# Kernel tuning notes

Measured on AMD Instinct MI355X. Metric: run time of the kernel, lower is better.

The kernel has to match this reference:

```python
import jax, jax.numpy as jnp
import numpy as np

D = 1024      # d_model
H = 8         # heads
DH = D // H
L = 12        # layers
E = 4         # experts
F = 2048      # dim_feedforward
NCLS = 10
SPARSITY = 0.5
EPS = 1e-5
B, S = 4, 512


def _xavier(key, shape):
    fan_in, fan_out = shape[-1], shape[-2] if len(shape) > 1 else shape[-1]
    scale = jnp.sqrt(2.0 / (fan_in + fan_out))
    return jax.random.normal(key, shape, jnp.float32) * scale


def setup_inputs() -> dict:
    key = jax.random.key(0)
    ks = jax.random.split(key, 16)
    return {
        "x": jax.random.normal(ks[0], (B, S, D), jnp.float32),
        "pos": jax.random.normal(ks[1], (1, 512, D), jnp.float32) * 0.02,
        # stacked per-layer transformer params
        "Wqkv": _xavier(ks[2], (L, 3 * D, D)), "bqkv": jnp.zeros((L, 3 * D), jnp.float32),
        "Wo": _xavier(ks[3], (L, D, D)),       "bo": jnp.zeros((L, D), jnp.float32),
        "ln1_s": jnp.ones((L, D), jnp.float32), "ln1_b": jnp.zeros((L, D), jnp.float32),
        "W1": _xavier(ks[4], (L, F, D)), "b1": jnp.zeros((L, F), jnp.float32),
        "W2": _xavier(ks[5], (L, D, F)), "b2": jnp.zeros((L, D), jnp.float32),
        "ln2_s": jnp.ones((L, D), jnp.float32), "ln2_b": jnp.zeros((L, D), jnp.float32),
        # shared gate / experts / classifier
        "Wg": _xavier(ks[6], (E, D)), "bg": jnp.zeros((E,), jnp.float32),
        "We": _xavier(ks[7], (E, D, D)), "be": jnp.zeros((E, D), jnp.float32),
        "Wf": _xavier(ks[8], (NCLS, D)), "bf": jnp.zeros((NCLS,), jnp.float32),
    }


def _layernorm(x, s, b):
    m = jnp.mean(x, axis=-1, keepdims=True)
    v = jnp.mean(jnp.square(x - m), axis=-1, keepdims=True)
    return (x - m) * jax.lax.rsqrt(v + EPS) * s + b


def _forward(x, pos, Wqkv, bqkv, Wo, bo, ln1_s, ln1_b, W1, b1, W2, b2,
             ln2_s, ln2_b, Wg, bg, We, be, Wf, bf):
    Bx, Sx, _ = x.shape
    x = x + pos[:, :Sx, :]
    for l in range(L):
        # --- self-attention (post-norm TransformerEncoderLayer, eval/no-dropout) ---
        qkv = x @ Wqkv[l].T + bqkv[l]                      # [B,S,3D]
        q, k, v = jnp.split(qkv, 3, axis=-1)
        q = q.reshape(Bx, Sx, H, DH).transpose(0, 2, 1, 3)  # bhsd
        k = k.reshape(Bx, Sx, H, DH).transpose(0, 2, 1, 3)
        v = v.reshape(Bx, Sx, H, DH).transpose(0, 2, 1, 3)
        attn = jax.nn.softmax(jnp.einsum('bhqd,bhkd->bhqk', q, k) / jnp.sqrt(jnp.float32(DH)), axis=-1)
        o = jnp.einsum('bhqk,bhkd->bhqd', attn, v).transpose(0, 2, 1, 3).reshape(Bx, Sx, D)
        o = o @ Wo[l].T + bo[l]
        x = _layernorm(x + o, ln1_s[l], ln1_b[l])
        # --- ffn (exact gelu) ---
        h = jax.nn.gelu(x @ W1[l].T + b1[l], approximate=False) @ W2[l].T + b2[l]
        x = _layernorm(x + h, ln2_s[l], ln2_b[l])
        # --- top-2 gated MoE (shared gate/experts across layers) ---
        gs = jax.nn.softmax(x @ Wg.T + bg, axis=-1)         # [B,S,E]
        vals, idx = jax.lax.top_k(gs, 2)                    # [B,S,2]
        all_out = jnp.einsum('bsd,eod->bseo', x, We) + be   # [B,S,E,D]
        sel = jnp.take_along_axis(all_out, idx[..., None], axis=2)  # [B,S,2,D]
        expert_out = jnp.sum(sel * vals[..., None], axis=2)
        x = x * (1.0 - SPARSITY) + expert_out * SPARSITY
    return x[:, -1, :] @ Wf.T + bf                          # [B,10]


def reference(x, pos, Wqkv, bqkv, Wo, bo, ln1_s, ln1_b, W1, b1, W2, b2,
              ln2_s, ln2_b, Wg, bg, We, be, Wf, bf):
    return _forward(x, pos, Wqkv, bqkv, Wo, bo, ln1_s, ln1_b, W1, b1, W2, b2,
                    ln2_s, ln2_b, Wg, bg, We, be, Wf, bf)
```

## Files before the change

### kernel.cpp

```cpp
#include <hip/hip_runtime.h>
#include <math.h>

#define D     1024
#define NH    8
#define DHD   128
#define NL    12
#define NE    4
#define FF    2048
#define NCLS  10
#define BB    4
#define SS    512
#define TT    (BB*SS)
#define EPSV  1e-5f
#define SPARS 0.5f

typedef __attribute__((ext_vector_type(8))) short bf16x8;
typedef __attribute__((ext_vector_type(4))) float f32x4;
typedef unsigned short ushortT;

__device__ __forceinline__ ushortT f2bf(float f) {
    unsigned u = __float_as_uint(f);
    u += 0x7FFF + ((u >> 16) & 1);
    return (ushortT)(u >> 16);
}
__device__ __forceinline__ float bf2f(ushortT h) {
    return __uint_as_float(((unsigned)h) << 16);
}

#define LDP 40

template<int MODE, int SK, int ACT, int BN>
__global__ __launch_bounds__(256)
void gemm_mfma(const ushortT* __restrict__ A, const float* __restrict__ Bw,
               const float* __restrict__ bias, void* __restrict__ Cv,
               int M, int N, int Ktot, int Klen, long eBw, long eBias, long eC)
{
    const int z = blockIdx.z;
    int koff = 0;
    float* Cf = nullptr; ushortT* Ch = nullptr;
    if constexpr (SK > 1) {
        koff = z * Klen;
        Cf = (float*)Cv + (size_t)z * M * N;
    } else {
        Bw   += (size_t)z * eBw;
        bias += (size_t)z * eBias;
        if constexpr (MODE == 0) Ch = (ushortT*)Cv + (size_t)z * eC;
        else                     Cf = (float*)Cv   + (size_t)z * eC;
    }

    constexpr int MR = (BN == 128) ? 4 : 2;
    __shared__ ushortT Asl[128 * LDP];
    __shared__ ushortT Bsl[BN * LDP];

    const int tid  = threadIdx.x;
    const int wave = tid >> 6, lane = tid & 63;
    const int wm = (BN == 128) ? (wave >> 1) * 64 : wave * 32;
    const int wn = (BN == 128) ? (wave & 1) * 64 : 0;
    const int fr = lane & 15;
    const int fq = lane >> 4;

    const int m0 = blockIdx.y * 128;
    const int n0 = blockIdx.x * BN;

    const int arow = tid >> 1;
    const int akc  = (tid & 1) * 2;
    const ushortT* Ag = A + (size_t)(m0 + arow) * Ktot + koff;
    const int srow = (BN == 128) ? (tid >> 3) : (tid >> 2);
    const int scb  = (BN == 128) ? (tid & 7) : (tid & 3);
    const float* Bg = Bw + (size_t)(n0 + srow) * Ktot + koff + scb * 4;

    f32x4 acc[MR][4] = {};

    for (int k0 = 0; k0 < Klen; k0 += 32) {
        bf16x8 av8[2];
        float4 bv[4];
        #pragma unroll
        for (int u = 0; u < 2; ++u)
            av8[u] = *reinterpret_cast<const bf16x8*>(Ag + k0 + (akc + u) * 8);
        if constexpr (BN == 128) {
            #pragma unroll
            for (int p = 0; p < 4; ++p)
                bv[p] = *reinterpret_cast<const float4*>(Bg + (size_t)(32*p) * Ktot + k0);
        } else {
            bv[0] = *reinterpret_cast<const float4*>(Bg + k0);
            bv[1] = *reinterpret_cast<const float4*>(Bg + k0 + 16);
        }
        __syncthreads();
        #pragma unroll
        for (int u = 0; u < 2; ++u)
            *reinterpret_cast<bf16x8*>(&Asl[arow*LDP + (akc + u)*8]) = av8[u];
        if constexpr (BN == 128) {
            #pragma unroll
            for (int p = 0; p < 4; ++p) {
                ushort4 b4; b4.x=f2bf(bv[p].x); b4.y=f2bf(bv[p].y); b4.z=f2bf(bv[p].z); b4.w=f2bf(bv[p].w);
                *reinterpret_cast<ushort4*>(&Bsl[(srow + 32*p)*LDP + scb*4]) = b4;
            }
        } else {
            ushort4 b0; b0.x=f2bf(bv[0].x); b0.y=f2bf(bv[0].y); b0.z=f2bf(bv[0].z); b0.w=f2bf(bv[0].w);
            ushort4 b1; b1.x=f2bf(bv[1].x); b1.y=f2bf(bv[1].y); b1.z=f2bf(bv[1].z); b1.w=f2bf(bv[1].w);
            *reinterpret_cast<ushort4*>(&Bsl[srow*LDP + scb*4])      = b0;
            *reinterpret_cast<ushort4*>(&Bsl[srow*LDP + scb*4 + 16]) = b1;
        }
        __syncthreads();

        bf16x8 af[MR], bfr[4];
        #pragma unroll
        for (int i = 0; i < MR; ++i)
            af[i]  = *reinterpret_cast<const bf16x8*>(&Asl[(wm + i*16 + fr)*LDP + fq*8]);
        #pragma unroll
        for (int j = 0; j < 4; ++j)
            bfr[j] = *reinterpret_cast<const bf16x8*>(&Bsl[(wn + j*16 + fr)*LDP + fq*8]);
        #pragma unroll
        for (int i = 0; i < MR; ++i)
            #pragma unroll
            for (int j = 0; j < 4; ++j)
                acc[i][j] = __builtin_amdgcn_mfma_f32_16x16x32_bf16(af[i], bfr[j], acc[i][j], 0, 0, 0);
    }

    #pragma unroll
    for (int j = 0; j < 4; ++j) {
        const int n = n0 + wn + j*16 + fr;
        float bb = 0.f;
        if constexpr (SK == 1) bb = bias[n];
        #pragma unroll
        for (int i = 0; i < MR; ++i) {
            const int mb = m0 + wm + i*16 + fq*4;
            if constexpr (SK > 1) {
                #pragma unroll
                for (int r = 0; r < 4; ++r)
                    Cf[(size_t)(mb + r) * N + n] = acc[i][j][r];
            } else if constexpr (MODE == 0) {
                #pragma unroll
                for (int r = 0; r < 4; ++r) {
                    float u = acc[i][j][r] + bb;
                    if constexpr (ACT == 1) u = 0.5f*u*(1.0f + erff(u*0.70710678118654752f));
                    Ch[(size_t)(mb + r) * N + n] = f2bf(u);
                }
            } else {
                #pragma unroll
                for (int r = 0; r < 4; ++r) {
                    float u = acc[i][j][r] + bb;
                    if constexpr (ACT == 1) u = 0.5f*u*(1.0f + erff(u*0.70710678118654752f));
                    Cf[(size_t)(mb + r) * N + n] = u;
                }
            }
        }
    }
}

__global__ __launch_bounds__(256)
void kv_prep(const float* __restrict__ qkv, ushortT* __restrict__ Kb, ushortT* __restrict__ Vt)
{
    __shared__ ushortT T[64*136];
    const int tid = threadIdx.x;
    const int st = blockIdx.x, bh = blockIdx.y;
    const int b = bh >> 3, h = bh & 7;
    const float* base = qkv + (size_t)(b*SS + st*64)*3*D + h*DHD;

    #pragma unroll
    for (int p = 0; p < 4; ++p) {
        const int row = (tid >> 4) + 16*p;
        const int colb = (tid & 15) * 8;
        {
            const float* src = base + (size_t)row*3*D + D + colb;
            float f[8];
            *reinterpret_cast<float4*>(f)   = *reinterpret_cast<const float4*>(src);
            *reinterpret_cast<float4*>(f+4) = *reinterpret_cast<const float4*>(src+4);
            bf16x8 u;
            #pragma unroll
            for (int e = 0; e < 8; ++e) ((ushortT*)&u)[e] = f2bf(f[e]);
            *reinterpret_cast<bf16x8*>(&Kb[((size_t)bh*SS + st*64 + row)*DHD + colb]) = u;
        }
        {
            const float* src = base + (size_t)row*3*D + 2*D + colb;
            float f[8];
            *reinterpret_cast<float4*>(f)   = *reinterpret_cast<const float4*>(src);
            *reinterpret_cast<float4*>(f+4) = *reinterpret_cast<const float4*>(src+4);
            #pragma unroll
            for (int e = 0; e < 8; ++e) T[row*136 + colb + e] = f2bf(f[e]);
        }
    }
    __syncthreads();
    #pragma unroll
    for (int p = 0; p < 4; ++p) {
        const int d  = (tid >> 3) + 32*p;
        const int sb = (tid & 7) * 8;
        bf16x8 u;
        #pragma unroll
        for (int e = 0; e < 8; ++e) ((ushortT*)&u)[e] = T[(sb + e)*136 + d];
        *reinterpret_cast<bf16x8*>(&Vt[((size_t)bh*DHD + d)*SS + st*64 + sb]) = u;
    }
}

#define KLP 136
#define VLP 72
#define PLP 72

__global__ __launch_bounds__(256)
void attn_mfma(const float* __restrict__ qkv, const ushortT* __restrict__ Kb,
               const ushortT* __restrict__ Vt, ushortT* __restrict__ o16)
{
    __shared__ ushortT Kl[64*KLP];
    __shared__ ushortT Vl[128*VLP];
    __shared__ ushortT Pl[4*16*PLP];

    const int tid = threadIdx.x;
    const int w = tid >> 6, lane = tid & 63;
    const int g = lane >> 4, c = lane & 15;
    const int bh = blockIdx.y;
    const int b = bh >> 3, h = bh & 7;
    const int q0 = blockIdx.x*64 + w*16;
    ushortT* Pw = Pl + w*16*PLP;

    bf16x8 qhi[4], qlo[4];
    const float scale = 0.08838834764831845f;
    {
        const float* Qrow = qkv + (size_t)(b*SS + q0 + c)*3*D + h*DHD;
        #pragma unroll
        for (int db = 0; db < 4; ++db) {
            float f[8];
            *reinterpret_cast<float4*>(f)   = *reinterpret_cast<const float4*>(Qrow + db*32 + g*8);
            *reinterpret_cast<float4*>(f+4) = *reinterpret_cast<const float4*>(Qrow + db*32 + g*8 + 4);
            #pragma unroll
            for (int e = 0; e < 8; ++e) {
                const float fs = f[e]*scale;
                const ushortT hi = f2bf(fs);
                ((ushortT*)&qhi[db])[e] = hi;
                ((ushortT*)&qlo[db])[e] = f2bf(fs - bf2f(hi));
            }
        }
    }

    const ushortT* Kg = Kb + (size_t)bh*SS*DHD;
    const ushortT* Vg = Vt + (size_t)bh*DHD*SS;

    float m_r[4], l_r[4];
    #pragma unroll
    for (int r = 0; r < 4; ++r) { m_r[r] = -1e30f; l_r[r] = 0.f; }
    f32x4 oacc[8] = {};

    for (int kt = 0; kt < SS/64; ++kt) {
        __syncthreads();
        #pragma unroll
        for (int p = 0; p < 4; ++p) {
            const int row = (tid >> 4) + 16*p;
            const int colb = (tid & 15)*8;
            bf16x8 u = *reinterpret_cast<const bf16x8*>(&Kg[(size_t)(kt*64 + row)*DHD + colb]);
            *reinterpret_cast<bf16x8*>(&Kl[row*KLP + colb]) = u;
        }
        #pragma unroll
        for (int p = 0; p < 4; ++p) {
            const int dr = (tid >> 3) + 32*p;
            const int sb = (tid & 7)*8;
            bf16x8 u = *reinterpret_cast<const bf16x8*>(&Vg[(size_t)dr*SS + kt*64 + sb]);
            *reinterpret_cast<bf16x8*>(&Vl[dr*VLP + sb]) = u;
        }
        __syncthreads();

        f32x4 s[4] = {};
        #pragma unroll
        for (int db = 0; db < 4; ++db) {
            bf16x8 kf[4];
            #pragma unroll
            for (int kb = 0; kb < 4; ++kb)
                kf[kb] = *reinterpret_cast<const bf16x8*>(&Kl[(kb*16 + c)*KLP + db*32 + g*8]);
            #pragma unroll
            for (int kb = 0; kb < 4; ++kb) {
                s[kb] = __builtin_amdgcn_mfma_f32_16x16x32_bf16(qhi[db], kf[kb], s[kb], 0, 0, 0);
                s[kb] = __builtin_amdgcn_mfma_f32_16x16x32_bf16(qlo[db], kf[kb], s[kb], 0, 0, 0);
            }
        }

        float tmax[4];
        #pragma unroll
        for (int r = 0; r < 4; ++r)
            tmax[r] = fmaxf(fmaxf(s[0][r], s[1][r]), fmaxf(s[2][r], s[3][r]));
        #pragma unroll
        for (int off = 1; off < 16; off <<= 1)
            #pragma unroll
            for (int r = 0; r < 4; ++r)
                tmax[r] = fmaxf(tmax[r], __shfl_xor(tmax[r], off));
        float mn[4], corr[4];
        #pragma unroll
        for (int r = 0; r < 4; ++r) {
            mn[r] = fmaxf(m_r[r], tmax[r]);
            corr[r] = __expf(m_r[r] - mn[r]);
            m_r[r] = mn[r];
        }
        float tsum[4] = {0.f, 0.f, 0.f, 0.f};
        #pragma unroll
        for (int kb = 0; kb < 4; ++kb)
            #pragma unroll
            for (int r = 0; r < 4; ++r) {
                const float p = __expf(s[kb][r] - mn[r]);
                s[kb][r] = p;
                tsum[r] += p;
            }
        #pragma unroll
        for (int off = 1; off < 16; off <<= 1)
            #pragma unroll
            for (int r = 0; r < 4; ++r)
                tsum[r] += __shfl_xor(tsum[r], off);
        #pragma unroll
        for (int r = 0; r < 4; ++r) l_r[r] = l_r[r]*corr[r] + tsum[r];
        #pragma unroll
        for (int df = 0; df < 8; ++df)
            #pragma unroll
            for (int r = 0; r < 4; ++r)
                oacc[df][r] *= corr[r];

        #pragma unroll
        for (int kb = 0; kb < 4; ++kb)
            #pragma unroll
            for (int r = 0; r < 4; ++r)
                Pw[(g*4 + r)*PLP + kb*16 + c] = f2bf(s[kb][r]);

        #pragma unroll
        for (int kk = 0; kk < 2; ++kk) {
            bf16x8 pa = *reinterpret_cast<const bf16x8*>(&Pw[c*PLP + kk*32 + g*8]);
            #pragma unroll
            for (int df = 0; df < 8; ++df) {
                bf16x8 vb = *reinterpret_cast<const bf16x8*>(&Vl[(df*16 + c)*VLP + kk*32 + g*8]);
                oacc[df] = __builtin_amdgcn_mfma_f32_16x16x32_bf16(pa, vb, oacc[df], 0, 0, 0);
            }
        }
    }

    #pragma unroll
    for (int r = 0; r < 4; ++r) {
        const float inv = 1.0f / l_r[r];
        ushortT* orow = o16 + (size_t)(b*SS + q0 + g*4 + r)*D + h*DHD + c;
        #pragma unroll
        for (int df = 0; df < 8; ++df)
            orow[df*16] = f2bf(oacc[df][r] * inv);
    }
}

template<int SK, int GATE>
__global__ __launch_bounds__(256)
void add_ln_r(const float* __restrict__ xin, const float* __restrict__ P,
              const float* __restrict__ dbias,
              const float* __restrict__ gs, const float* __restrict__ gb,
              float* __restrict__ x32, ushortT* __restrict__ x16,
              const float* __restrict__ Wg, const float* __restrict__ bg,
              float* __restrict__ gv, int* __restrict__ gi)
{
    const int row = blockIdx.x, tid = threadIdx.x;
    const size_t off = (size_t)row*D + tid*4;
    float4 a = *reinterpret_cast<const float4*>(xin + off);
    float d0, d1, d2, d3;
    {
        float4 bvd = *reinterpret_cast<const float4*>(dbias + tid*4);
        d0 = bvd.x; d1 = bvd.y; d2 = bvd.z; d3 = bvd.w;
    }
    #pragma unroll
    for (int s = 0; s < SK; ++s) {
        float4 pv = *reinterpret_cast<const float4*>(P + (size_t)s*TT*D + off);
        d0 += pv.x; d1 += pv.y; d2 += pv.z; d3 += pv.w;
    }
    float v0=a.x+d0, v1=a.y+d1, v2=a.z+d2, v3=a.w+d3;
    __shared__ float red[2][4];
    float s = v0+v1+v2+v3;
    #pragma unroll
    for (int o = 32; o; o >>= 1) s += __shfl_xor(s, o, 64);
    if ((tid & 63) == 0) red[0][tid>>6] = s;
    __syncthreads();
    const float mean = (red[0][0]+red[0][1]+red[0][2]+red[0][3]) * (1.0f/D);
    v0-=mean; v1-=mean; v2-=mean; v3-=mean;
    float qv = v0*v0+v1*v1+v2*v2+v3*v3;
    #pragma unroll
    for (int o = 32; o; o >>= 1) qv += __shfl_xor(qv, o, 64);
    if ((tid & 63) == 0) red[1][tid>>6] = qv;
    __syncthreads();
    const float var = (red[1][0]+red[1][1]+red[1][2]+red[1][3]) * (1.0f/D);
    const float rstd = rsqrtf(var + EPSV);
    float4 sv = *reinterpret_cast<const float4*>(gs + tid*4);
    float4 bv = *reinterpret_cast<const float4*>(gb + tid*4);
    float ov[4];
    ov[0] = v0*rstd*sv.x + bv.x;
    ov[1] = v1*rstd*sv.y + bv.y;
    ov[2] = v2*rstd*sv.z + bv.z;
    ov[3] = v3*rstd*sv.w + bv.w;
    float4 o4; o4.x=ov[0]; o4.y=ov[1]; o4.z=ov[2]; o4.w=ov[3];
    *reinterpret_cast<float4*>(x32 + off) = o4;
    ushort4 h4; h4.x=f2bf(ov[0]); h4.y=f2bf(ov[1]); h4.z=f2bf(ov[2]); h4.w=f2bf(ov[3]);
    *reinterpret_cast<ushort4*>(x16 + off) = h4;

    if constexpr (GATE) {
        float p[4] = {0.f, 0.f, 0.f, 0.f};
        #pragma unroll
        for (int e = 0; e < 4; ++e) {
            const float* wr = Wg + (size_t)e*D + tid*4;
            p[e] = ov[0]*wr[0] + ov[1]*wr[1] + ov[2]*wr[2] + ov[3]*wr[3];
        }
        #pragma unroll
        for (int o = 32; o; o >>= 1) {
            p[0] += __shfl_xor(p[0], o, 64); p[1] += __shfl_xor(p[1], o, 64);
            p[2] += __shfl_xor(p[2], o, 64); p[3] += __shfl_xor(p[3], o, 64);
        }
        __shared__ float gred[4][4];
        if ((tid & 63) == 0) {
            const int w = tid>>6;
            gred[w][0]=p[0]; gred[w][1]=p[1]; gred[w][2]=p[2]; gred[w][3]=p[3];
        }
        __syncthreads();
        if (tid == 0) {
            float g[4];
            #pragma unroll
            for (int e = 0; e < 4; ++e) g[e] = gred[0][e]+gred[1][e]+gred[2][e]+gred[3][e] + bg[e];
            const float mx = fmaxf(fmaxf(g[0],g[1]), fmaxf(g[2],g[3]));
            float ssum = 0.f;
            #pragma unroll
            for (int e = 0; e < 4; ++e) { g[e] = __expf(g[e]-mx); ssum += g[e]; }
            const float inv = 1.0f/ssum;
            #pragma unroll
            for (int e = 0; e < 4; ++e) g[e] *= inv;
            int i0 = 0;
            for (int e = 1; e < 4; ++e) if (g[e] > g[i0]) i0 = e;
            int i1 = (i0 == 0) ? 1 : 0;
            for (int e = 0; e < 4; ++e) if (e != i0 && g[e] > g[i1]) i1 = e;
            gv[row*2]   = g[i0]; gv[row*2+1] = g[i1];
            gi[row*2]   = i0;    gi[row*2+1] = i1;
        }
    }
}

__global__ __launch_bounds__(256)
void moe_combine(float* __restrict__ x, ushortT* __restrict__ x16,
                 const float* __restrict__ eo,
                 const float* __restrict__ gv, const int* __restrict__ gi)
{
    const size_t i = (size_t)blockIdx.x*256 + threadIdx.x;
    const int t = (int)(i >> 10);
    const float w0 = gv[t*2]*SPARS, w1 = gv[t*2+1]*SPARS;
    const size_t TD = (size_t)TT*D;
    const float e0 = eo[(size_t)gi[t*2]*TD + i];
    const float e1 = eo[(size_t)gi[t*2+1]*TD + i];
    const float r = x[i]*(1.0f-SPARS) + w0*e0 + w1*e1;
    x[i] = r;
    x16[i] = f2bf(r);
}

__global__ __launch_bounds__(256)
void addpos(const float* __restrict__ xin, const float* __restrict__ pos,
            float* __restrict__ xo, ushortT* __restrict__ x16)
{
    const size_t i = (size_t)blockIdx.x*256 + threadIdx.x;
    const float r = xin[i] + pos[i & ((size_t)SS*D - 1)];
    xo[i] = r;
    x16[i] = f2bf(r);
}

__global__ __launch_bounds__(64)
void final_kernel(const float* __restrict__ x, const float* __restrict__ Wf,
                  const float* __restrict__ bf, float* __restrict__ out)
{
    const int b = blockIdx.x / NCLS, n = blockIdx.x % NCLS;
    const float* xr = x + ((size_t)b*SS + SS-1)*D;
    const int tid = threadIdx.x;
    float s = 0.f;
    for (int d = tid; d < D; d += 64) s += xr[d]*Wf[(size_t)n*D + d];
    #pragma unroll
    for (int o = 32; o; o >>= 1) s += __shfl_xor(s, o, 64);
    if (tid == 0) out[b*NCLS + n] = s + bf[n];
}

extern "C" void kernel_launch(void* const* d_in, const int* in_sizes, int n_in,
                              void* d_out, int out_size, void* d_ws, size_t ws_size,
                              hipStream_t stream)
{
    const float* x_in = (const float*)d_in[0];
    const float* pos  = (const float*)d_in[1];
    const float* Wqkv = (const float*)d_in[2];
    const float* bqkv = (const float*)d_in[3];
    const float* Wo   = (const float*)d_in[4];
    const float* bo   = (const float*)d_in[5];
    const float* ln1s = (const float*)d_in[6];
    const float* ln1b = (const float*)d_in[7];
    const float* W1   = (const float*)d_in[8];
    const float* b1   = (const float*)d_in[9];
    const float* W2   = (const float*)d_in[10];
    const float* b2   = (const float*)d_in[11];
    const float* ln2s = (const float*)d_in[12];
    const float* ln2b = (const float*)d_in[13];
    const float* Wg   = (const float*)d_in[14];
    const float* bg   = (const float*)d_in[15];
    const float* We   = (const float*)d_in[16];
    const float* be   = (const float*)d_in[17];
    const float* Wf   = (const float*)d_in[18];
    const float* bf   = (const float*)d_in[19];
    float* out = (float*)d_out;

    float* ws     = (float*)d_ws;
    float*   xbuf  = ws;
    ushortT* xb16  = (ushortT*)(xbuf + (size_t)TT*D);
    ushortT* ob16  = xb16 + (size_t)TT*D;
    float*   scratch = (float*)(ob16 + (size_t)TT*D);
    ushortT* hb16 = (ushortT*)(scratch + (size_t)TT*D*4);
    float*   gv    = (float*)(hb16 + (size_t)TT*FF);
    int*     gi    = (int*)(gv + (size_t)TT*2);
    float*   qkvbuf = scratch;
    ushortT* Kb     = (ushortT*)(qkvbuf + (size_t)TT*3*D);
    ushortT* Vt     = Kb + (size_t)BB*NH*SS*DHD;
    float*   parts  = scratch;
    float*   ebuf   = scratch;

    const dim3 blk(256);
    addpos<<<dim3(TT*D/256), blk, 0, stream>>>(x_in, pos, xbuf, xb16);

    for (int l = 0; l < NL; ++l) {
        gemm_mfma<1,1,0,64><<<dim3(3*D/64, TT/128, 1), blk, 0, stream>>>(
            xb16, Wqkv + (size_t)l*3*D*D, bqkv + (size_t)l*3*D, qkvbuf,
            TT, 3*D, D, D, 0, 0, 0);
        kv_prep<<<dim3(SS/64, BB*NH), blk, 0, stream>>>(qkvbuf, Kb, Vt);
        attn_mfma<<<dim3(SS/64, BB*NH), blk, 0, stream>>>(qkvbuf, Kb, Vt, ob16);
        gemm_mfma<1,4,0,128><<<dim3(D/128, TT/128, 4), blk, 0, stream>>>(
            ob16, Wo + (size_t)l*D*D, bo, parts, TT, D, D, D/4, 0, 0, 0);
        add_ln_r<4,0><<<dim3(TT), blk, 0, stream>>>(
            xbuf, parts, bo + (size_t)l*D, ln1s + (size_t)l*D, ln1b + (size_t)l*D,
            xbuf, xb16, nullptr, nullptr, nullptr, nullptr);
        gemm_mfma<0,1,1,64><<<dim3(FF/64, TT/128, 1), blk, 0, stream>>>(
            xb16, W1 + (size_t)l*FF*D, b1 + (size_t)l*FF, hb16, TT, FF, D, D, 0, 0, 0);
        gemm_mfma<1,4,0,128><<<dim3(D/128, TT/128, 4), blk, 0, stream>>>(
            hb16, W2 + (size_t)l*D*FF, b2, parts, TT, D, FF, FF/4, 0, 0, 0);
        add_ln_r<4,1><<<dim3(TT), blk, 0, stream>>>(
            xbuf, parts, b2 + (size_t)l*D, ln2s + (size_t)l*D, ln2b + (size_t)l*D,
            xbuf, xb16, Wg, bg, gv, gi);
        gemm_mfma<1,1,0,64><<<dim3(D/64, TT/128, NE), blk, 0, stream>>>(
            xb16, We, be, ebuf, TT, D, D, D, (long)D*D, (long)D, (long)TT*D);
        moe_combine<<<dim3(TT*D/256), blk, 0, stream>>>(xbuf, xb16, ebuf, gv, gi);
    }
    final_kernel<<<dim3(BB*NCLS), dim3(64), 0, stream>>>(xbuf, Wf, bf, out);
}
```

Measured before the change: 2.735 ms.

## Route tokens to top-2 experts and run sparse expert GEMM over gathered slots

The dense MoE expert GEMM, which computed all four experts for every token, becomes a routed one. The gate kernel now uses atomics to build per-expert token lists and a token-to-slot map. The expert GEMM gathers A rows through the slot list and exits early for tiles past each expert's count. The combine kernel reads outputs by slot. This cuts expert FLOPs roughly in half. In exchange it adds atomics, indirect row loads and nondeterministic slot ordering, and it relies on the existing epilogue writing to row m0+r, which indexes slots.

```diff
diff --git a/kernel.cpp b/kernel.cpp
--- a/kernel.cpp
+++ b/kernel.cpp
@@ -29,13 +29,23 @@
 
 #define LDP 40
 
-template<int MODE, int SK, int ACT, int BN>
+template<int MODE, int SK, int ACT, int BN, int EPI>
 __global__ __launch_bounds__(256)
 void gemm_mfma(const ushortT* __restrict__ A, const float* __restrict__ Bw,
                const float* __restrict__ bias, void* __restrict__ Cv,
-               int M, int N, int Ktot, int Klen, long eBw, long eBias, long eC)
+               int M, int N, int Ktot, int Klen, long eBw, long eBias, long eC,
+               const int* __restrict__ slotTok, const int* __restrict__ cnt)
 {
     const int z = blockIdx.z;
+    const int m0 = blockIdx.y * 128;
+    const int n0 = blockIdx.x * BN;
+
+    int cntE = 0;
+    if constexpr (EPI == 2) {
+        cntE = cnt[z];
+        if (m0 >= cntE) return;
+    }
+
     int koff = 0;
     float* Cf = nullptr; ushortT* Ch = nullptr;
     if constexpr (SK > 1) {
@@ -59,12 +69,16 @@
     const int fr = lane & 15;
     const int fq = lane >> 4;
 
-    const int m0 = blockIdx.y * 128;
-    const int n0 = blockIdx.x * BN;
-
     const int arow = tid >> 1;
     const int akc  = (tid & 1) * 2;
-    const ushortT* Ag = A + (size_t)(m0 + arow) * Ktot + koff;
+    const ushortT* Ag;
+    if constexpr (EPI == 2) {
+        const int rsl = m0 + arow;
+        const int tok = (rsl < cntE) ? slotTok[(size_t)z*TT + rsl] : 0;
+        Ag = A + (size_t)tok * Ktot;
+    } else {
+        Ag = A + (size_t)(m0 + arow) * Ktot + koff;
+    }
     const int srow = (BN == 128) ? (tid >> 3) : (tid >> 2);
     const int scb  = (BN == 128) ? (tid & 7) : (tid & 3);
     const float* Bg = Bw + (size_t)(n0 + srow) * Ktot + koff + scb * 4;
@@ -343,7 +357,8 @@
               const float* __restrict__ gs, const float* __restrict__ gb,
               float* __restrict__ x32, ushortT* __restrict__ x16,
               const float* __restrict__ Wg, const float* __restrict__ bg,
-              float* __restrict__ gv, int* __restrict__ gi)
+              float* __restrict__ gv, int* __restrict__ slotTok,
+              int* __restrict__ tokSlot, int* __restrict__ cntL)
 {
     const int row = blockIdx.x, tid = threadIdx.x;
     const size_t off = (size_t)row*D + tid*4;
@@ -420,7 +435,12 @@
             int i1 = (i0 == 0) ? 1 : 0;
             for (int e = 0; e < 4; ++e) if (e != i0 && g[e] > g[i1]) i1 = e;
             gv[row*2]   = g[i0]; gv[row*2+1] = g[i1];
-            gi[row*2]   = i0;    gi[row*2+1] = i1;
+            const int p0 = atomicAdd(&cntL[i0], 1);
+            slotTok[i0*TT + p0] = row;
+            const int p1 = atomicAdd(&cntL[i1], 1);
+            slotTok[i1*TT + p1] = row;
+            tokSlot[row*2]   = i0*TT + p0;
+            tokSlot[row*2+1] = i1*TT + p1;
         }
     }
 }
@@ -428,14 +448,14 @@
 __global__ __launch_bounds__(256)
 void moe_combine(float* __restrict__ x, ushortT* __restrict__ x16,
                  const float* __restrict__ eo,
-                 const float* __restrict__ gv, const int* __restrict__ gi)
+                 const float* __restrict__ gv, const int* __restrict__ tokSlot)
 {
     const size_t i = (size_t)blockIdx.x*256 + threadIdx.x;
     const int t = (int)(i >> 10);
+    const int col = (int)(i & 1023);
     const float w0 = gv[t*2]*SPARS, w1 = gv[t*2+1]*SPARS;
-    const size_t TD = (size_t)TT*D;
-    const float e0 = eo[(size_t)gi[t*2]*TD + i];
-    const float e1 = eo[(size_t)gi[t*2+1]*TD + i];
+    const float e0 = eo[(size_t)tokSlot[t*2]  *D + col];
+    const float e1 = eo[(size_t)tokSlot[t*2+1]*D + col];
     const float r = x[i]*(1.0f-SPARS) + w0*e0 + w1*e1;
     x[i] = r;
     x16[i] = f2bf(r);
@@ -449,6 +469,12 @@
     const float r = xin[i] + pos[i & ((size_t)SS*D - 1)];
     xo[i] = r;
     x16[i] = f2bf(r);
+}
+
+__global__ __launch_bounds__(64)
+void zero_cnt(int* __restrict__ cnt)
+{
+    if (threadIdx.x < NL*NE) cnt[threadIdx.x] = 0;
 }
 
 __global__ __launch_bounds__(64)
@@ -498,37 +524,44 @@
     float*   scratch = (float*)(ob16 + (size_t)TT*D);
     ushortT* hb16 = (ushortT*)(scratch + (size_t)TT*D*4);
     float*   gv    = (float*)(hb16 + (size_t)TT*FF);
-    int*     gi    = (int*)(gv + (size_t)TT*2);
+    int*     tokSlot = (int*)(gv + (size_t)TT*2);
+    int*     slotTok = tokSlot + (size_t)TT*2;
+    int*     cnt     = slotTok + (size_t)NE*TT;
     float*   qkvbuf = scratch;
     ushortT* Kb     = (ushortT*)(qkvbuf + (size_t)TT*3*D);
     ushortT* Vt     = Kb + (size_t)BB*NH*SS*DHD;
     float*   parts  = scratch;
-    float*   ebuf   = scratch;
+    float*   slotOut = scratch;
 
     const dim3 blk(256);
+    zero_cnt<<<dim3(1), dim3(64), 0, stream>>>(cnt);
     addpos<<<dim3(TT*D/256), blk, 0, stream>>>(x_in, pos, xbuf, xb16);
 
     for (int l = 0; l < NL; ++l) {
-        gemm_mfma<1,1,0,64><<<dim3(3*D/64, TT/128, 1), blk, 0, stream>>>(
+        gemm_mfma<1,1,0,64,0><<<dim3(3*D/64, TT/128, 1), blk, 0, stream>>>(
             xb16, Wqkv + (size_t)l*3*D*D, bqkv + (size_t)l*3*D, qkvbuf,
-            TT, 3*D, D, D, 0, 0, 0);
+            TT, 3*D, D, D, 0, 0, 0, nullptr, nullptr);
         kv_prep<<<dim3(SS/64, BB*NH), blk, 0, stream>>>(qkvbuf, Kb, Vt);
         attn_mfma<<<dim3(SS/64, BB*NH), blk, 0, stream>>>(qkvbuf, Kb, Vt, ob16);
-        gemm_mfma<1,4,0,128><<<dim3(D/128, TT/128, 4), blk, 0, stream>>>(
-            ob16, Wo + (size_t)l*D*D, bo, parts, TT, D, D, D/4, 0, 0, 0);
+        gemm_mfma<1,4,0,128,0><<<dim3(D/128, TT/128, 4), blk, 0, stream>>>(
+            ob16, Wo + (size_t)l*D*D, bo, parts, TT, D, D, D/4, 0, 0, 0,
+            nullptr, nullptr);
         add_ln_r<4,0><<<dim3(TT), blk, 0, stream>>>(
             xbuf, parts, bo + (size_t)l*D, ln1s + (size_t)l*D, ln1b + (size_t)l*D,
-            xbuf, xb16, nullptr, nullptr, nullptr, nullptr);
-        gemm_mfma<0,1,1,64><<<dim3(FF/64, TT/128, 1), blk, 0, stream>>>(
-            xb16, W1 + (size_t)l*FF*D, b1 + (size_t)l*FF, hb16, TT, FF, D, D, 0, 0, 0);
-        gemm_mfma<1,4,0,128><<<dim3(D/128, TT/128, 4), blk, 0, stream>>>(
-            hb16, W2 + (size_t)l*D*FF, b2, parts, TT, D, FF, FF/4, 0, 0, 0);
+            xbuf, xb16, nullptr, nullptr, nullptr, nullptr, nullptr, nullptr);
+        gemm_mfma<0,1,1,64,0><<<dim3(FF/64, TT/128, 1), blk, 0, stream>>>(
+            xb16, W1 + (size_t)l*FF*D, b1 + (size_t)l*FF, hb16, TT, FF, D, D, 0, 0, 0,
+            nullptr, nullptr);
+        gemm_mfma<1,4,0,128,0><<<dim3(D/128, TT/128, 4), blk, 0, stream>>>(
+            hb16, W2 + (size_t)l*D*FF, b2, parts, TT, D, FF, FF/4, 0, 0, 0,
+            nullptr, nullptr);
         add_ln_r<4,1><<<dim3(TT), blk, 0, stream>>>(
             xbuf, parts, b2 + (size_t)l*D, ln2s + (size_t)l*D, ln2b + (size_t)l*D,
-            xbuf, xb16, Wg, bg, gv, gi);
-        gemm_mfma<1,1,0,64><<<dim3(D/64, TT/128, NE), blk, 0, stream>>>(
-            xb16, We, be, ebuf, TT, D, D, D, (long)D*D, (long)D, (long)TT*D);
-        moe_combine<<<dim3(TT*D/256), blk, 0, stream>>>(xbuf, xb16, ebuf, gv, gi);
+            xbuf, xb16, Wg, bg, gv, slotTok, tokSlot, cnt + l*NE);
+        gemm_mfma<1,1,0,64,2><<<dim3(D/64, TT/128, NE), blk, 0, stream>>>(
+            xb16, We, be, slotOut, TT, D, D, D, (long)D*D, (long)D, (long)TT*D,
+            slotTok, cnt + l*NE);
+        moe_combine<<<dim3(TT*D/256), blk, 0, stream>>>(xbuf, xb16, slotOut, gv, tokSlot);
     }
     final_kernel<<<dim3(BB*NCLS), dim3(64), 0, stream>>>(xbuf, Wf, bf, out);
 }
```

Result: slower. 3.256 ms (+19.1%).
